# Performance work log

Hardware: AMD Instinct MI355X
Metric: run time of the kernel (lower is better)

Reference implementation:

```python
import jax, jax.numpy as jnp
import numpy as np

HIDDEN = 1024
HEADS = 16
HEAD_DIM = HIDDEN // HEADS
SCALE = 1.0 / (HEAD_DIM ** 0.5)


def setup_inputs() -> dict:
    key = jax.random.key(0)
    k1, k2, k3 = jax.random.split(key, 3)
    B, S = 2, 2048
    x = jax.random.normal(k1, (B, S, HIDDEN), dtype=jnp.float32)
    # torch Linear weights: (out_features, in_features), y = x @ W.T
    qkv_w = jax.random.normal(k2, (3 * HIDDEN, HIDDEN), dtype=jnp.float32) * (HIDDEN ** -0.5)
    out_w = jax.random.normal(k3, (HIDDEN, HIDDEN), dtype=jnp.float32) * (HIDDEN ** -0.5)
    return {"x": x, "qkv_w": qkv_w, "out_w": out_w}


def reference(x, qkv_w, out_w):
    B, S, H = x.shape
    qkv = jnp.einsum('bsh,oh->bso', x, qkv_w)  # [B,S,3H]
    q, k, v = jnp.split(qkv, 3, axis=-1)
    def heads(t):
        return t.reshape(B, S, HEADS, HEAD_DIM).transpose(0, 2, 1, 3)  # [B,nh,S,hd]
    q, k, v = heads(q), heads(k), heads(v)
    scores = jnp.einsum('bhqd,bhkd->bhqk', q, k) * SCALE  # [B,nh,S,S]
    attn = jax.nn.softmax(scores, axis=-1)
    out = jnp.einsum('bhqk,bhkd->bhqd', attn, v)  # [B,nh,S,hd]
    out = out.transpose(0, 2, 1, 3).reshape(B, S, H)
    return jnp.einsum('bsh,oh->bso', out, out_w)
```

## Files before the change

kernel.cpp:

```cpp
#include <hip/hip_runtime.h>
#include <hip/hip_bf16.h>

#define BB 2
#define SS 2048
#define HH 1024
#define NH 16
#define HD 64
#define MM (BB * SS)
#define N_QKV (3 * HH)
#define KK HH

typedef __attribute__((ext_vector_type(8))) short short8;
typedef __attribute__((ext_vector_type(4))) float floatx4;
typedef __attribute__((ext_vector_type(16))) float floatx16;

#define MFMA16(a, b, c) __builtin_amdgcn_mfma_f32_16x16x32_bf16(a, b, c, 0, 0, 0)
#define MFMA32(a, b, c) __builtin_amdgcn_mfma_f32_32x32x16_bf16(a, b, c, 0, 0, 0)

__device__ __forceinline__ unsigned short f2bf(float f) {
  unsigned int u = __builtin_bit_cast(unsigned int, f);
  u += 0x7FFFu + ((u >> 16) & 1u);
  return (unsigned short)(u >> 16);
}

__device__ __forceinline__ float fexp2(float x) {
#if __has_builtin(__builtin_amdgcn_exp2f)
  return __builtin_amdgcn_exp2f(x);
#else
  float r; asm("v_exp_f32 %0, %1" : "=v"(r) : "v"(x)); return r;
#endif
}

__device__ __forceinline__ unsigned int pack2e(float lo, float hi) {
  unsigned int a = __builtin_bit_cast(unsigned int, lo) + 0x8000u;
  unsigned int b = __builtin_bit_cast(unsigned int, hi) + 0x8000u;
  return __builtin_amdgcn_perm(b, a, 0x07060302u);
}

__device__ __forceinline__ unsigned int cvtpk(float lo, float hi) {
  unsigned int r;
  asm("v_cvt_pk_bf16_f32 %0, %1, %2" : "=v"(r) : "v"(lo), "v"(hi));
  return r;
}

__device__ __forceinline__ uint4 cvt8pk(float4 lo, float4 hi) {
  uint4 u;
  u.x = cvtpk(lo.x, lo.y);
  u.y = cvtpk(lo.z, lo.w);
  u.z = cvtpk(hi.x, hi.y);
  u.w = cvtpk(hi.z, hi.w);
  return u;
}

__device__ __forceinline__ void gload_lds16(const void* g, void* l) {
  __builtin_amdgcn_global_load_lds((const __attribute__((address_space(1))) void*)g,
                                   (__attribute__((address_space(3))) void*)l,
                                   16, 0, 0);
}

__global__ __launch_bounds__(256) void cast_all(const float* __restrict__ x,
                                                const float* __restrict__ w1,
                                                const float* __restrict__ w2,
                                                unsigned short* __restrict__ xb,
                                                unsigned short* __restrict__ w1b,
                                                unsigned short* __restrict__ w2b) {
  const int NX = MM * KK / 8;
  const int NW1 = N_QKV * KK / 8;
  int i = blockIdx.x * 256 + threadIdx.x;
  const float* s; unsigned short* d; int o;
  if (i < NX)            { s = x;  d = xb;  o = i; }
  else if (i < NX + NW1) { s = w1; d = w1b; o = i - NX; }
  else                   { s = w2; d = w2b; o = i - (NX + NW1); }
  float4 lo = *(const float4*)(s + (size_t)o * 8);
  float4 hi = *(const float4*)(s + (size_t)o * 8 + 4);
  *(uint4*)(d + (size_t)o * 8) = cvt8pk(lo, hi);
}

__global__ __launch_bounds__(256) void cast_g(const float* __restrict__ s,
                                              unsigned short* __restrict__ d) {
  size_t i = (size_t)blockIdx.x * 256 + threadIdx.x;
  float4 lo = *(const float4*)(s + i * 8);
  float4 hi = *(const float4*)(s + i * 8 + 4);
  *(uint4*)(d + i * 8) = cvt8pk(lo, hi);
}

__global__ __launch_bounds__(256) void gemm_qkv_dma(const unsigned short* __restrict__ Xb,
                                                    const unsigned short* __restrict__ Wb,
                                                    unsigned short* __restrict__ qb,
                                                    unsigned short* __restrict__ kb,
                                                    unsigned short* __restrict__ vtb) {
  __shared__ __attribute__((aligned(16))) unsigned short As[2][128 * 64];
  __shared__ __attribute__((aligned(16))) unsigned short Bs[2][128 * 64];
  const int tid = threadIdx.x;
  const int wave = tid >> 6, lane = tid & 63;
  const int quad = lane >> 4, lc = lane & 15;
  const int wg = (blockIdx.x & 7) * 96 + (blockIdx.x >> 3);
  const int m0 = (wg / 24) * 128, n0 = (wg % 24) * 128;
  const int wm = (wave >> 1) * 64, wn = (wave & 1) * 64;

  floatx4 acc[4][4];
#pragma unroll
  for (int i = 0; i < 4; i++)
#pragma unroll
    for (int j = 0; j < 4; j++) acc[i][j] = (floatx4){0.f, 0.f, 0.f, 0.f};

  const int srow = lane >> 3;
  const int schk = (lane & 7) ^ srow;
  const unsigned short* Ab = Xb + (size_t)(m0 + wave * 8 + srow) * KK + schk * 8;
  const unsigned short* Bb = Wb + (size_t)(n0 + wave * 8 + srow) * KK + schk * 8;

#define STAGEQ(buf, k0)                                                          \
  do {                                                                           \
    _Pragma("unroll")                                                            \
    for (int g = 0; g < 4; g++) {                                                \
      gload_lds16(Ab + (size_t)g * 32 * KK + (k0), &As[buf][(g * 32 + wave * 8) * 64]); \
      gload_lds16(Bb + (size_t)g * 32 * KK + (k0), &Bs[buf][(g * 32 + wave * 8) * 64]); \
    }                                                                            \
  } while (0)

  STAGEQ(0, 0);

  const int NIT = KK / 64;
  for (int it = 0; it < NIT; ++it) {
    const int cb = it & 1;
    if (it + 1 < NIT) {
      STAGEQ(cb ^ 1, (it + 1) * 64);
      asm volatile("s_waitcnt vmcnt(8)" ::: "memory");
    } else {
      asm volatile("s_waitcnt vmcnt(0)" ::: "memory");
    }
    __builtin_amdgcn_s_barrier();
    __builtin_amdgcn_sched_barrier(0);
    __builtin_amdgcn_s_setprio(1);
#pragma unroll
    for (int kk = 0; kk < 2; kk++) {
      short8 af[4], bfr[4];
#pragma unroll
      for (int i = 0; i < 4; i++) {
        const int cs = ((kk * 4 + quad) ^ (lc & 7)) << 3;
        af[i]  = *(const short8*)(&As[cb][(wm + i * 16 + lc) * 64 + cs]);
        bfr[i] = *(const short8*)(&Bs[cb][(wn + i * 16 + lc) * 64 + cs]);
      }
#pragma unroll
      for (int i = 0; i < 4; i++)
#pragma unroll
        for (int j = 0; j < 4; j++) acc[i][j] = MFMA16(af[i], bfr[j], acc[i][j]);
    }
    __builtin_amdgcn_s_setprio(0);
    __builtin_amdgcn_sched_barrier(0);
    __builtin_amdgcn_s_barrier();
  }
#undef STAGEQ

  const float QSCALE = 0.125f * 1.44269504f;
#pragma unroll
  for (int j = 0; j < 4; j++) {
    int n = n0 + wn + j * 16 + lc;
#pragma unroll
    for (int i = 0; i < 4; i++) {
      int mbase = m0 + wm + i * 16 + quad * 4;
      int b = mbase >> 11;
      int s0 = mbase & 2047;
      if (n < HH) {
        int h = n >> 6, d = n & 63;
#pragma unroll
        for (int r = 0; r < 4; r++)
          qb[(((size_t)(b * NH + h) * SS + s0 + r) * HD) + d] = f2bf(acc[i][j][r] * QSCALE);
      } else if (n < 2 * HH) {
        int n2 = n - HH; int h = n2 >> 6, d = n2 & 63;
#pragma unroll
        for (int r = 0; r < 4; r++)
          kb[(((size_t)(b * NH + h) * SS + s0 + r) * HD) + d] = f2bf(acc[i][j][r]);
      } else {
        int n2 = n - 2 * HH; int h = n2 >> 6, d = n2 & 63;
        ushort4 p;
        p.x = f2bf(acc[i][j][0]); p.y = f2bf(acc[i][j][1]);
        p.z = f2bf(acc[i][j][2]); p.w = f2bf(acc[i][j][3]);
        *(ushort4*)(vtb + ((size_t)(b * NH + h) * HD + d) * SS + s0) = p;
      }
    }
  }
}

__global__ __launch_bounds__(256) void gemm_qkv_f32(const unsigned short* __restrict__ Xb,
                                                    const float* __restrict__ Wf,
                                                    unsigned short* __restrict__ qb,
                                                    unsigned short* __restrict__ kb,
                                                    unsigned short* __restrict__ vtb) {
  __shared__ __attribute__((aligned(16))) unsigned short As[128 * 32];
  __shared__ __attribute__((aligned(16))) unsigned short Bs[128 * 32];
  const int tid = threadIdx.x;
  const int wave = tid >> 6, lane = tid & 63;
  const int quad = lane >> 4, lc = lane & 15;
  const int m0 = blockIdx.y * 128, n0 = blockIdx.x * 128;
  const int wm = (wave >> 1) * 64, wn = (wave & 1) * 64;
  const int sr = tid >> 2, sc = (tid & 3) * 8;

  floatx4 acc[4][4];
#pragma unroll
  for (int i = 0; i < 4; i++)
#pragma unroll
    for (int j = 0; j < 4; j++) acc[i][j] = (floatx4){0.f, 0.f, 0.f, 0.f};

  const unsigned short* Axp = Xb + (size_t)(m0 + sr) * KK + sc;
  unsigned short* AsD = As + wave * 512;
  const float* Bg = Wf + (size_t)(n0 + sr) * KK + sc;
  unsigned short* BsW = Bs + wave * 512 + lane * 8;
  float4 b0l = *(const float4*)(Bg),                    b0h = *(const float4*)(Bg + 4);
  float4 b1l = *(const float4*)(Bg + (size_t)64 * KK),  b1h = *(const float4*)(Bg + (size_t)64 * KK + 4);

  for (int it = 0; it < KK / 32; ++it) {
    const int k0 = it * 32;
    __syncthreads();
    gload_lds16(Axp + k0, AsD);
    gload_lds16(Axp + (size_t)64 * KK + k0, AsD + 2048);
    *(uint4*)(BsW) = cvt8pk(b0l, b0h);
    *(uint4*)(BsW + 2048) = cvt8pk(b1l, b1h);
    if (it + 1 < KK / 32) {
      b0l = *(const float4*)(Bg + k0 + 32);                    b0h = *(const float4*)(Bg + k0 + 36);
      b1l = *(const float4*)(Bg + k0 + 32 + (size_t)64 * KK);  b1h = *(const float4*)(Bg + k0 + 36 + (size_t)64 * KK);
    }
    __syncthreads();
    short8 af[4], bfr[4];
#pragma unroll
    for (int i = 0; i < 4; i++) {
      af[i]  = *(const short8*)(As + (wm + i * 16 + lc) * 32 + quad * 8);
      bfr[i] = *(const short8*)(Bs + (wn + i * 16 + lc) * 32 + quad * 8);
    }
#pragma unroll
    for (int i = 0; i < 4; i++)
#pragma unroll
      for (int j = 0; j < 4; j++) acc[i][j] = MFMA16(af[i], bfr[j], acc[i][j]);
  }

  const float QSCALE = 0.125f * 1.44269504f;
#pragma unroll
  for (int j = 0; j < 4; j++) {
    int n = n0 + wn + j * 16 + lc;
#pragma unroll
    for (int i = 0; i < 4; i++) {
      int mbase = m0 + wm + i * 16 + quad * 4;
      int b = mbase >> 11;
      int s0 = mbase & 2047;
      if (n < HH) {
        int h = n >> 6, d = n & 63;
#pragma unroll
        for (int r = 0; r < 4; r++)
          qb[(((size_t)(b * NH + h) * SS + s0 + r) * HD) + d] = f2bf(acc[i][j][r] * QSCALE);
      } else if (n < 2 * HH) {
        int n2 = n - HH; int h = n2 >> 6, d = n2 & 63;
#pragma unroll
        for (int r = 0; r < 4; r++)
          kb[(((size_t)(b * NH + h) * SS + s0 + r) * HD) + d] = f2bf(acc[i][j][r]);
      } else {
        int n2 = n - 2 * HH; int h = n2 >> 6, d = n2 & 63;
        ushort4 p;
        p.x = f2bf(acc[i][j][0]); p.y = f2bf(acc[i][j][1]);
        p.z = f2bf(acc[i][j][2]); p.w = f2bf(acc[i][j][3]);
        *(ushort4*)(vtb + ((size_t)(b * NH + h) * HD + d) * SS + s0) = p;
      }
    }
  }
}

__device__ __forceinline__ int co(int row, int c16) {
  return row * 64 + ((c16 ^ ((row ^ (row >> 3)) & 7)) << 3);
}

__global__ __launch_bounds__(256, 2) void attn_kernel(const unsigned short* __restrict__ qg,
                                                      const unsigned short* __restrict__ kg,
                                                      const unsigned short* __restrict__ vtg,
                                                      unsigned short* __restrict__ og) {
  __shared__ __attribute__((aligned(16))) unsigned short Sall[16384];
  unsigned short* Qs = Sall;
  unsigned short* Ks = Sall + 8192;
  unsigned short* Vs = Sall + 12288;

  const int tid = threadIdx.x;
  const int w = tid >> 6, lane = tid & 63;
  const int hl = lane >> 5, c = lane & 31;
  const int q0 = blockIdx.x * 128;
  const int head = blockIdx.y, b = blockIdx.z;

  const unsigned short* qbase = qg + (size_t)(b * NH + head) * SS * HD;
  const unsigned short* kbase = kg + (size_t)(b * NH + head) * SS * HD;
  const unsigned short* vbase = vtg + (size_t)(b * NH + head) * HD * SS;

  {
    int row = tid >> 3, cc = tid & 7;
#pragma unroll
    for (int s = 0; s < 4; s++)
      *(uint4*)(Qs + co(row + 32 * s, cc)) =
          *(const uint4*)(qbase + (size_t)(q0 + row + 32 * s) * HD + cc * 8);
  }

  const int frow = tid >> 3, fc = tid & 7;
  uint4 k0r = *(const uint4*)(kbase + (size_t)frow * HD + fc * 8);
  uint4 k1r = *(const uint4*)(kbase + (size_t)(frow + 32) * HD + fc * 8);
  uint4 v0r = *(const uint4*)(vbase + (size_t)frow * SS + fc * 8);
  uint4 v1r = *(const uint4*)(vbase + (size_t)(frow + 32) * SS + fc * 8);

  floatx16 oacc0, oacc1, lacc;
#pragma unroll
  for (int i = 0; i < 16; i++) { oacc0[i] = 0.f; oacc1[i] = 0.f; lacc[i] = 0.f; }

  short8 ones;
#pragma unroll
  for (int i = 0; i < 8; i++) ones[i] = (short)0x3F80;

  short8 qa[4];

  for (int kt = 0; kt < SS; kt += 64) {
    __syncthreads();
    *(uint4*)(Ks + co(frow, fc)) = k0r;
    *(uint4*)(Ks + co(frow + 32, fc)) = k1r;
    *(uint4*)(Vs + co(frow, fc)) = v0r;
    *(uint4*)(Vs + co(frow + 32, fc)) = v1r;
    if (kt + 64 < SS) {
      k0r = *(const uint4*)(kbase + (size_t)(kt + 64 + frow) * HD + fc * 8);
      k1r = *(const uint4*)(kbase + (size_t)(kt + 96 + frow) * HD + fc * 8);
      v0r = *(const uint4*)(vbase + (size_t)frow * SS + kt + 64 + fc * 8);
      v1r = *(const uint4*)(vbase + (size_t)(frow + 32) * SS + kt + 64 + fc * 8);
    }
    __syncthreads();

    if (kt == 0) {
#pragma unroll
      for (int ks = 0; ks < 4; ks++)
        qa[ks] = *(const short8*)(Qs + co(w * 32 + c, ks * 2 + hl));
    }

    floatx16 sacc0, sacc1;
#pragma unroll
    for (int i = 0; i < 16; i++) { sacc0[i] = 0.f; sacc1[i] = 0.f; }
    __builtin_amdgcn_s_setprio(1);
#pragma unroll
    for (int ks = 0; ks < 4; ks++) {
      short8 ka0 = *(const short8*)(Ks + co(c, ks * 2 + hl));
      short8 ka1 = *(const short8*)(Ks + co(32 + c, ks * 2 + hl));
      sacc0 = MFMA32(ka0, qa[ks], sacc0);
      sacc1 = MFMA32(ka1, qa[ks], sacc1);
    }
    __builtin_amdgcn_s_setprio(0);

    short8 pb[4];
#pragma unroll
    for (int kb = 0; kb < 4; kb++) {
      const floatx16& s = (kb < 2) ? sacc0 : sacc1;
      int base = (kb & 1) * 8;
      unsigned int u0 = pack2e(fexp2(s[base + 0]), fexp2(s[base + 1]));
      unsigned int u1 = pack2e(fexp2(s[base + 2]), fexp2(s[base + 3]));
      unsigned int u2 = pack2e(fexp2(s[base + 4]), fexp2(s[base + 5]));
      unsigned int u3 = pack2e(fexp2(s[base + 6]), fexp2(s[base + 7]));
      uint4 u = {u0, u1, u2, u3};
      pb[kb] = __builtin_bit_cast(short8, u);
    }

    __builtin_amdgcn_s_setprio(1);
#pragma unroll
    for (int kb = 0; kb < 4; kb++) {
      uint2 lo0 = *(const uint2*)(Vs + co(c, 2 * kb) + 4 * hl);
      uint2 hi0 = *(const uint2*)(Vs + co(c, 2 * kb + 1) + 4 * hl);
      uint4 a0 = {lo0.x, lo0.y, hi0.x, hi0.y};
      short8 va0 = __builtin_bit_cast(short8, a0);
      uint2 lo1 = *(const uint2*)(Vs + co(32 + c, 2 * kb) + 4 * hl);
      uint2 hi1 = *(const uint2*)(Vs + co(32 + c, 2 * kb + 1) + 4 * hl);
      uint4 a1 = {lo1.x, lo1.y, hi1.x, hi1.y};
      short8 va1 = __builtin_bit_cast(short8, a1);
      oacc0 = MFMA32(va0, pb[kb], oacc0);
      oacc1 = MFMA32(va1, pb[kb], oacc1);
      lacc = MFMA32(ones, pb[kb], lacc);
    }
    __builtin_amdgcn_s_setprio(0);
  }

  __syncthreads();
  unsigned short* sc = Sall + w * 2176;
  float inv = 1.0f / lacc[0];
#pragma unroll
  for (int t = 0; t < 8; t++) {
    int d0 = ((2 * t) & 3) + 8 * (t >> 1) + 4 * hl;
    *(unsigned int*)(sc + c * 68 + d0) = pack2e(oacc0[2 * t] * inv, oacc0[2 * t + 1] * inv);
    *(unsigned int*)(sc + c * 68 + 32 + d0) = pack2e(oacc1[2 * t] * inv, oacc1[2 * t + 1] * inv);
  }
  {
    int ql = lane >> 1, hf = lane & 1;
    size_t row = (size_t)(b * SS + q0 + w * 32 + ql);
    unsigned short* dst = og + row * HH + head * 64 + hf * 32;
    const unsigned short* srcp = sc + ql * 68 + hf * 32;
#pragma unroll
    for (int s = 0; s < 4; s++) {
      uint2 a = *(const uint2*)(srcp + s * 8);
      uint2 bq = *(const uint2*)(srcp + s * 8 + 4);
      uint4 v = {a.x, a.y, bq.x, bq.y};
      *(uint4*)(dst + s * 8) = v;
    }
  }
}

__global__ __launch_bounds__(256) void gemm_out_dma(const unsigned short* __restrict__ A,
                                                    const unsigned short* __restrict__ Wb,
                                                    float* __restrict__ C) {
  __shared__ __attribute__((aligned(16))) unsigned short As[2][128 * 64];
  __shared__ __attribute__((aligned(16))) unsigned short Bs[2][64 * 64];
  const int tid = threadIdx.x;
  const int wave = tid >> 6, lane = tid & 63;
  const int quad = lane >> 4, lc = lane & 15;
  const int wg = (blockIdx.x & 7) * 64 + (blockIdx.x >> 3);
  const int m0 = (wg / 16) * 128, n0 = (wg % 16) * 64;
  const int wm = (wave >> 1) * 64, wn = (wave & 1) * 32;

  floatx4 acc[4][2];
#pragma unroll
  for (int i = 0; i < 4; i++)
#pragma unroll
    for (int j = 0; j < 2; j++) acc[i][j] = (floatx4){0.f, 0.f, 0.f, 0.f};

  const int srow = lane >> 3;
  const int schk = (lane & 7) ^ srow;
  const unsigned short* Ab = A  + (size_t)(m0 + wave * 8 + srow) * KK + schk * 8;
  const unsigned short* Bb = Wb + (size_t)(n0 + wave * 8 + srow) * KK + schk * 8;

#define STAGEO(buf, k0)                                                          \
  do {                                                                           \
    _Pragma("unroll")                                                            \
    for (int g = 0; g < 4; g++)                                                  \
      gload_lds16(Ab + (size_t)g * 32 * KK + (k0), &As[buf][(g * 32 + wave * 8) * 64]); \
    _Pragma("unroll")                                                            \
    for (int g = 0; g < 2; g++)                                                  \
      gload_lds16(Bb + (size_t)g * 32 * KK + (k0), &Bs[buf][(g * 32 + wave * 8) * 64]); \
  } while (0)

  STAGEO(0, 0);

  const int NIT = KK / 64;
  for (int it = 0; it < NIT; ++it) {
    const int cb = it & 1;
    if (it + 1 < NIT) {
      STAGEO(cb ^ 1, (it + 1) * 64);
      asm volatile("s_waitcnt vmcnt(6)" ::: "memory");
    } else {
      asm volatile("s_waitcnt vmcnt(0)" ::: "memory");
    }
    __builtin_amdgcn_s_barrier();
    __builtin_amdgcn_sched_barrier(0);
    __builtin_amdgcn_s_setprio(1);
#pragma unroll
    for (int kk = 0; kk < 2; kk++) {
      short8 af[4], bfr[2];
#pragma unroll
      for (int i = 0; i < 4; i++)
        af[i] = *(const short8*)(&As[cb][(wm + i * 16 + lc) * 64 + (((kk * 4 + quad) ^ (lc & 7)) << 3)]);
#pragma unroll
      for (int j = 0; j < 2; j++)
        bfr[j] = *(const short8*)(&Bs[cb][(wn + j * 16 + lc) * 64 + (((kk * 4 + quad) ^ (lc & 7)) << 3)]);
#pragma unroll
      for (int i = 0; i < 4; i++)
#pragma unroll
        for (int j = 0; j < 2; j++) acc[i][j] = MFMA16(af[i], bfr[j], acc[i][j]);
    }
    __builtin_amdgcn_s_setprio(0);
    __builtin_amdgcn_sched_barrier(0);
    __builtin_amdgcn_s_barrier();
  }
#undef STAGEO

#pragma unroll
  for (int i = 0; i < 4; i++)
#pragma unroll
    for (int j = 0; j < 2; j++) {
      int m = m0 + wm + i * 16 + quad * 4;
      int n = n0 + wn + j * 16 + lc;
#pragma unroll
      for (int r = 0; r < 4; r++) C[(size_t)(m + r) * HH + n] = acc[i][j][r];
    }
}

extern "C" void kernel_launch(void* const* d_in, const int* in_sizes, int n_in,
                              void* d_out, int out_size, void* d_ws, size_t ws_size,
                              hipStream_t stream) {
  const float* x = (const float*)d_in[0];
  const float* qkv_w = (const float*)d_in[1];
  const float* out_w = (const float*)d_in[2];
  float* out = (float*)d_out;

  char* ws = (char*)d_ws;
  unsigned short* qb  = (unsigned short*)(ws + 0);
  unsigned short* kb  = (unsigned short*)(ws + 8388608);
  unsigned short* vtb = (unsigned short*)(ws + 16777216);
  unsigned short* xb  = (unsigned short*)(ws + 25165824);
  unsigned short* ao  = xb;

  const bool big = ws_size >= 40ull * 1024 * 1024;
  unsigned short* w1b = big ? (unsigned short*)(ws + 33554432) : nullptr;
  unsigned short* w2b = big ? (unsigned short*)(ws + 39845888) : nullptr;

  if (big) {
    cast_all<<<dim3(4096), dim3(256), 0, stream>>>(x, qkv_w, out_w, xb, w1b, w2b);
    gemm_qkv_dma<<<dim3(768), dim3(256), 0, stream>>>(xb, w1b, qb, kb, vtb);
    attn_kernel<<<dim3(SS / 128, NH, BB), dim3(256), 0, stream>>>(qb, kb, vtb, ao);
    gemm_out_dma<<<dim3(512), dim3(256), 0, stream>>>(ao, w2b, out);
  } else {
    unsigned short* wob = qb;
    cast_g<<<dim3(MM * KK / 2048), dim3(256), 0, stream>>>(x, xb);
    gemm_qkv_f32<<<dim3(N_QKV / 128, MM / 128), dim3(256), 0, stream>>>(xb, qkv_w, qb, kb, vtb);
    attn_kernel<<<dim3(SS / 128, NH, BB), dim3(256), 0, stream>>>(qb, kb, vtb, ao);
    cast_g<<<dim3(HH * KK / 2048), dim3(256), 0, stream>>>(out_w, wob);
    gemm_out_dma<<<dim3(512), dim3(256), 0, stream>>>(ao, wob, out);
  }
}
```

Before: 182.1 us.

## Double-buffer K/V tiles in LDS with one barrier per iteration

The attention kernel now keeps two K/V tile buffers in shared memory. Each iteration writes the next tile's registers into the alternate buffer and issues global loads two tiles ahead, then computes on the current buffer. The two __syncthreads per iteration become a single waitcnt plus barrier at the end. Shared memory per block grows from 32KB to 48KB, which could limit occupancy at two blocks per CU, and register pressure may rise slightly.

```diff
diff --git a/kernel.cpp b/kernel.cpp
--- a/kernel.cpp
+++ b/kernel.cpp
@@ -271,10 +271,8 @@
                                                       const unsigned short* __restrict__ kg,
                                                       const unsigned short* __restrict__ vtg,
                                                       unsigned short* __restrict__ og) {
-  __shared__ __attribute__((aligned(16))) unsigned short Sall[16384];
+  __shared__ __attribute__((aligned(16))) unsigned short Sall[24576];
   unsigned short* Qs = Sall;
-  unsigned short* Ks = Sall + 8192;
-  unsigned short* Vs = Sall + 12288;
 
   const int tid = threadIdx.x;
   const int w = tid >> 6, lane = tid & 63;
@@ -299,6 +297,18 @@
   uint4 k1r = *(const uint4*)(kbase + (size_t)(frow + 32) * HD + fc * 8);
   uint4 v0r = *(const uint4*)(vbase + (size_t)frow * SS + fc * 8);
   uint4 v1r = *(const uint4*)(vbase + (size_t)(frow + 32) * SS + fc * 8);
+  {
+    unsigned short* K0 = Sall + 8192;
+    unsigned short* V0 = Sall + 16384;
+    *(uint4*)(K0 + co(frow, fc)) = k0r;
+    *(uint4*)(K0 + co(frow + 32, fc)) = k1r;
+    *(uint4*)(V0 + co(frow, fc)) = v0r;
+    *(uint4*)(V0 + co(frow + 32, fc)) = v1r;
+  }
+  k0r = *(const uint4*)(kbase + (size_t)(64 + frow) * HD + fc * 8);
+  k1r = *(const uint4*)(kbase + (size_t)(96 + frow) * HD + fc * 8);
+  v0r = *(const uint4*)(vbase + (size_t)frow * SS + 64 + fc * 8);
+  v1r = *(const uint4*)(vbase + (size_t)(frow + 32) * SS + 64 + fc * 8);
 
   floatx16 oacc0, oacc1, lacc;
 #pragma unroll
@@ -308,26 +318,33 @@
 #pragma unroll
   for (int i = 0; i < 8; i++) ones[i] = (short)0x3F80;
 
+  asm volatile("s_waitcnt lgkmcnt(0)" ::: "memory");
+  __builtin_amdgcn_s_barrier();
+  __builtin_amdgcn_sched_barrier(0);
+
   short8 qa[4];
+#pragma unroll
+  for (int ks = 0; ks < 4; ks++)
+    qa[ks] = *(const short8*)(Qs + co(w * 32 + c, ks * 2 + hl));
 
   for (int kt = 0; kt < SS; kt += 64) {
-    __syncthreads();
-    *(uint4*)(Ks + co(frow, fc)) = k0r;
-    *(uint4*)(Ks + co(frow + 32, fc)) = k1r;
-    *(uint4*)(Vs + co(frow, fc)) = v0r;
-    *(uint4*)(Vs + co(frow + 32, fc)) = v1r;
+    const int cur = (kt >> 6) & 1;
+    unsigned short* Kc = Sall + 8192 + cur * 4096;
+    unsigned short* Vc = Sall + 16384 + cur * 4096;
+
     if (kt + 64 < SS) {
-      k0r = *(const uint4*)(kbase + (size_t)(kt + 64 + frow) * HD + fc * 8);
-      k1r = *(const uint4*)(kbase + (size_t)(kt + 96 + frow) * HD + fc * 8);
-      v0r = *(const uint4*)(vbase + (size_t)frow * SS + kt + 64 + fc * 8);
-      v1r = *(const uint4*)(vbase + (size_t)(frow + 32) * SS + kt + 64 + fc * 8);
-    }
-    __syncthreads();
-
-    if (kt == 0) {
-#pragma unroll
-      for (int ks = 0; ks < 4; ks++)
-        qa[ks] = *(const short8*)(Qs + co(w * 32 + c, ks * 2 + hl));
+      unsigned short* Kn = Sall + 8192 + (cur ^ 1) * 4096;
+      unsigned short* Vn = Sall + 16384 + (cur ^ 1) * 4096;
+      *(uint4*)(Kn + co(frow, fc)) = k0r;
+      *(uint4*)(Kn + co(frow + 32, fc)) = k1r;
+      *(uint4*)(Vn + co(frow, fc)) = v0r;
+      *(uint4*)(Vn + co(frow + 32, fc)) = v1r;
+      if (kt + 128 < SS) {
+        k0r = *(const uint4*)(kbase + (size_t)(kt + 128 + frow) * HD + fc * 8);
+        k1r = *(const uint4*)(kbase + (size_t)(kt + 160 + frow) * HD + fc * 8);
+        v0r = *(const uint4*)(vbase + (size_t)frow * SS + kt + 128 + fc * 8);
+        v1r = *(const uint4*)(vbase + (size_t)(frow + 32) * SS + kt + 128 + fc * 8);
+      }
     }
 
     floatx16 sacc0, sacc1;
@@ -336,8 +353,8 @@
     __builtin_amdgcn_s_setprio(1);
 #pragma unroll
     for (int ks = 0; ks < 4; ks++) {
-      short8 ka0 = *(const short8*)(Ks + co(c, ks * 2 + hl));
-      short8 ka1 = *(const short8*)(Ks + co(32 + c, ks * 2 + hl));
+      short8 ka0 = *(const short8*)(Kc + co(c, ks * 2 + hl));
+      short8 ka1 = *(const short8*)(Kc + co(32 + c, ks * 2 + hl));
       sacc0 = MFMA32(ka0, qa[ks], sacc0);
       sacc1 = MFMA32(ka1, qa[ks], sacc1);
     }
@@ -359,12 +376,12 @@
     __builtin_amdgcn_s_setprio(1);
 #pragma unroll
     for (int kb = 0; kb < 4; kb++) {
-      uint2 lo0 = *(const uint2*)(Vs + co(c, 2 * kb) + 4 * hl);
-      uint2 hi0 = *(const uint2*)(Vs + co(c, 2 * kb + 1) + 4 * hl);
+      uint2 lo0 = *(const uint2*)(Vc + co(c, 2 * kb) + 4 * hl);
+      uint2 hi0 = *(const uint2*)(Vc + co(c, 2 * kb + 1) + 4 * hl);
       uint4 a0 = {lo0.x, lo0.y, hi0.x, hi0.y};
       short8 va0 = __builtin_bit_cast(short8, a0);
-      uint2 lo1 = *(const uint2*)(Vs + co(32 + c, 2 * kb) + 4 * hl);
-      uint2 hi1 = *(const uint2*)(Vs + co(32 + c, 2 * kb + 1) + 4 * hl);
+      uint2 lo1 = *(const uint2*)(Vc + co(32 + c, 2 * kb) + 4 * hl);
+      uint2 hi1 = *(const uint2*)(Vc + co(32 + c, 2 * kb + 1) + 4 * hl);
       uint4 a1 = {lo1.x, lo1.y, hi1.x, hi1.y};
       short8 va1 = __builtin_bit_cast(short8, a1);
       oacc0 = MFMA32(va0, pb[kb], oacc0);
@@ -372,9 +389,12 @@
       lacc = MFMA32(ones, pb[kb], lacc);
     }
     __builtin_amdgcn_s_setprio(0);
-  }
-
-  __syncthreads();
+
+    asm volatile("s_waitcnt lgkmcnt(0)" ::: "memory");
+    __builtin_amdgcn_s_barrier();
+    __builtin_amdgcn_sched_barrier(0);
+  }
+
   unsigned short* sc = Sall + w * 2176;
   float inv = 1.0f / lacc[0];
 #pragma unroll
```

Result: no change. 185.3 us (+1.8%).
